# Performance work log

Hardware: AMD Instinct MI355X
Metric: run time of the kernel (lower is better)

Reference implementation:

```python
import jax, jax.numpy as jnp
import numpy as np

WS = 8          # window size
NH = 12         # num heads
DEPTH = 2       # blocks: W-MSA, SW-MSA
EPS = 1e-6
N = WS * WS     # tokens per window


def _rel_index():
    c = np.stack(np.meshgrid(np.arange(WS), np.arange(WS), indexing='ij')).reshape(2, -1)
    rel = (c[:, :, None] - c[:, None, :]).transpose(1, 2, 0)
    rel[:, :, 0] += WS - 1
    rel[:, :, 1] += WS - 1
    rel[:, :, 0] *= 2 * WS - 1
    return rel.sum(-1)  # [N, N] int

REL_IDX = jnp.asarray(_rel_index())


def _shift_mask(H, W, shift):
    # static (numpy) construction, H/W/shift are Python ints
    img = np.zeros((H, W))
    cnt = 0
    for hs in (slice(0, -WS), slice(-WS, -shift), slice(-shift, None)):
        for wsl in (slice(0, -WS), slice(-WS, -shift), slice(-shift, None)):
            img[hs, wsl] = cnt
            cnt += 1
    win = img.reshape(H // WS, WS, W // WS, WS).transpose(0, 2, 1, 3).reshape(-1, N)
    diff = win[:, None, :] - win[:, :, None]
    return jnp.asarray(np.where(diff != 0, -100.0, 0.0), jnp.float32)  # [nW, N, N]


def _ln(x):
    m = x.mean(-1, keepdims=True)
    v = ((x - m) ** 2).mean(-1, keepdims=True)
    return (x - m) * jax.lax.rsqrt(v + EPS)


def _block(x, H, W, emb, p, shift):
    qkv_w, qkv_b, proj_w, proj_b, ff1_w, ff1_b, ff2_w, ff2_b, ada_w, ada_b, bias_table = p
    B, L, C = x.shape
    hd = C // NH
    ada = jax.nn.silu(emb) @ ada_w.T + ada_b  # [B, 6C]
    sh_sa, sc_sa, g_sa, sh_ff, sc_ff, g_ff = jnp.split(ada, 6, axis=-1)
    h = _ln(x) * (1.0 + sc_sa[:, None]) + sh_sa[:, None]
    h = h.reshape(B, H, W, C)
    if shift > 0:
        h = jnp.roll(h, (-shift, -shift), (1, 2))
    # window partition -> [B*nW, N, C]
    win = h.reshape(B, H // WS, WS, W // WS, WS, C).transpose(0, 1, 3, 2, 4, 5).reshape(-1, N, C)
    B_ = win.shape[0]
    qkv = (win @ qkv_w.T + qkv_b).reshape(B_, N, 3, NH, hd)
    q, k, v = qkv[:, :, 0], qkv[:, :, 1], qkv[:, :, 2]
    attn = jnp.einsum('bnhd,bmhd->bhnm', q, k) * (hd ** -0.5)
    bias = bias_table[REL_IDX]  # [N, N, NH]
    attn = attn + bias.transpose(2, 0, 1)[None]
    if shift > 0:
        mask = _shift_mask(H, W, shift)  # [nW, N, N]
        nW = mask.shape[0]
        attn = (attn.reshape(B, nW, NH, N, N) + mask[None, :, None]).reshape(B_, NH, N, N)
    attn = jax.nn.softmax(attn, axis=-1)
    out = jnp.einsum('bhnm,bmhd->bnhd', attn, v).reshape(B_, N, C)
    out = out @ proj_w.T + proj_b
    # window reverse
    h = out.reshape(B, H // WS, W // WS, WS, WS, C).transpose(0, 1, 3, 2, 4, 5).reshape(B, H, W, C)
    if shift > 0:
        h = jnp.roll(h, (shift, shift), (1, 2))
    x = x + g_sa[:, None] * h.reshape(B, L, C)
    h2 = _ln(x) * (1.0 + sc_ff[:, None]) + sh_ff[:, None]
    ff = jax.nn.gelu(h2 @ ff1_w.T + ff1_b, approximate=False) @ ff2_w.T + ff2_b
    return x + g_ff[:, None] * ff


def _forward(x, emb, H, W, params):
    for i in range(DEPTH):
        p = tuple(a[i] for a in params)
        x = _block(x, H, W, emb, p, 0 if i % 2 == 0 else WS // 2)
    return x


def setup_inputs() -> dict:
    key = jax.random.key(0)
    ks = jax.random.split(key, 16)
    C, E, FF = 384, 384, 4 * 384
    B, H, W = 8, 64, 64
    p = lambda k, shape: jax.random.normal(k, shape, jnp.float32) * 0.02
    return {
        'x': jax.random.normal(ks[0], (B, H * W, C), jnp.float32),
        'H': H,
        'W': W,
        'emb': jax.random.normal(ks[1], (B, E), jnp.float32),
        'qkv_w': p(ks[2], (DEPTH, 3 * C, C)),
        'qkv_b': p(ks[3], (DEPTH, 3 * C)),
        'proj_w': p(ks[4], (DEPTH, C, C)),
        'proj_b': p(ks[5], (DEPTH, C)),
        'ff1_w': p(ks[6], (DEPTH, FF, C)),
        'ff1_b': p(ks[7], (DEPTH, FF)),
        'ff2_w': p(ks[8], (DEPTH, C, FF)),
        'ff2_b': p(ks[9], (DEPTH, C)),
        'ada_w': p(ks[10], (DEPTH, 6 * C, E)),
        'ada_b': p(ks[11], (DEPTH, 6 * C)),
        'bias_table': p(ks[12], (DEPTH, (2 * WS - 1) ** 2, NH)),
    }


def reference(x, H, W, emb, qkv_w, qkv_b, proj_w, proj_b, ff1_w, ff1_b, ff2_w, ff2_b, ada_w, ada_b, bias_table):
    params = (qkv_w, qkv_b, proj_w, proj_b, ff1_w, ff1_b, ff2_w, ff2_b, ada_w, ada_b, bias_table)
    return _forward(x, emb, H, W, params)
```

## Files before the change

kernel.cpp:

```cpp
#include <hip/hip_runtime.h>

typedef __bf16 bf16_t;
typedef bf16_t bf16x8 __attribute__((ext_vector_type(8)));
typedef float f32x4 __attribute__((ext_vector_type(4)));

#define EPI_STORE 0
#define EPI_GELU 1
#define EPI_RES_WIN 2
#define EPI_RES_ID 3

__device__ __forceinline__ float bf2f(unsigned short u) {
    union { unsigned int i; float f; } x; x.i = ((unsigned int)u) << 16; return x.f;
}
__device__ __forceinline__ unsigned short f2bf(float f) {
    union { __bf16 h; unsigned short u; } c; c.h = (__bf16)f; return c.u;
}
__device__ __forceinline__ float gelu_f(float v) {
    float u = v * (0.7978845608f + 0.0356774081f * v * v);
    return v / (1.0f + __expf(-2.0f * u));
}

__device__ __forceinline__ void async_cp16(const unsigned short* g, unsigned short* l) {
    __builtin_amdgcn_global_load_lds(
        (const __attribute__((address_space(1))) unsigned int*)g,
        (__attribute__((address_space(3))) unsigned int*)l, 16, 0, 0);
}

__device__ __forceinline__ int map_win(int m, int shift) {
    int n = m & 63, w = m >> 6;
    int b = w >> 6, ww = w & 63;
    int hh = ((ww >> 3) * 8 + (n >> 3) + shift) & 63;
    int wc = ((ww & 7) * 8 + (n & 7) + shift) & 63;
    return (b << 12) + (hh << 6) + wc;
}


__global__ void f2bf_kernel(const float* __restrict__ in,
                            unsigned short* __restrict__ out, int n) {
    int i = blockIdx.x * 256 + threadIdx.x;
    if (i < n) out[i] = f2bf(in[i]);
}

__global__ void silu_kernel(const float* __restrict__ emb,
                            float* __restrict__ out, int n) {
    int i = blockIdx.x * 256 + threadIdx.x;
    if (i < n) { float e = emb[i]; out[i] = e / (1.0f + expf(-e)); }
}

__global__ __launch_bounds__(64) void ada_kernel(
    const float* __restrict__ se,
    const float* __restrict__ ada_w,
    const float* __restrict__ ada_b,
    float* __restrict__ ada_out)
{
    int j = blockIdx.x;
    int layer = blockIdx.y;
    int t = threadIdx.x;
    const float* wr = ada_w + ((long)layer * 2304 + j) * 384;
    float w[6];
#pragma unroll
    for (int q = 0; q < 6; q++) w[q] = wr[t + 64 * q];
    float bias = ada_b[layer * 2304 + j];
    for (int b = 0; b < 8; b++) {
        float p = 0.f;
#pragma unroll
        for (int q = 0; q < 6; q++) p += se[b * 384 + t + 64 * q] * w[q];
#pragma unroll
        for (int o = 32; o > 0; o >>= 1) p += __shfl_xor(p, o);
        if (t == 0) ada_out[((long)layer * 8 + b) * 2304 + j] = p + bias;
    }
}

__global__ __launch_bounds__(256) void ln_mod_kernel(
    const float* __restrict__ x, const float* __restrict__ ada,
    unsigned short* __restrict__ h, int sh_off, int sc_off)
{
    int row = blockIdx.x * 4 + (threadIdx.x >> 6);
    int b = row >> 12;
    int t = threadIdx.x & 63;
    const float* xr = x + (long)row * 384;
    float v[6];
    float s = 0.f;
#pragma unroll
    for (int j = 0; j < 6; j++) { v[j] = xr[t + 64 * j]; s += v[j]; }
#pragma unroll
    for (int o = 32; o > 0; o >>= 1) s += __shfl_xor(s, o);
    float mean = s * (1.0f / 384.0f);
    float s2 = 0.f;
#pragma unroll
    for (int j = 0; j < 6; j++) { float d = v[j] - mean; s2 += d * d; }
#pragma unroll
    for (int o = 32; o > 0; o >>= 1) s2 += __shfl_xor(s2, o);
    float rstd = rsqrtf(s2 * (1.0f / 384.0f) + 1e-6f);
    const float* adab = ada + (long)b * 2304;
#pragma unroll
    for (int j = 0; j < 6; j++) {
        int c = t + 64 * j;
        float val = (v[j] - mean) * rstd * (1.0f + adab[sc_off + c]) + adab[sh_off + c];
        h[(long)row * 384 + c] = f2bf(val);
    }
}


template <int EPI, bool GATHER, bool RESINIT>
__global__ __launch_bounds__(256) void gemm128(
    const unsigned short* __restrict__ A,
    const unsigned short* __restrict__ W,
    const float* __restrict__ bias,
    unsigned short* __restrict__ out,
    float* __restrict__ xres,
    const float* __restrict__ xbase,
    const float* __restrict__ gvec,
    int M, int N, int K, int shift)
{
    __shared__ __align__(16) unsigned short As[128 * 64];
    __shared__ __align__(16) unsigned short Bs[128 * 64];

    const int tid = threadIdx.x;
    const int wv = tid >> 6, lane = tid & 63;
    const int m0 = blockIdx.y * 128, n0 = blockIdx.x * 128;

    const int r8 = lane >> 3;
    const int cofs = ((lane & 7) ^ r8) * 8;
    long arow[4], brow[4];
#pragma unroll
    for (int t = 0; t < 4; t++) {
        int rl = wv * 32 + t * 8 + r8;
        arow[t] = GATHER ? (long)map_win(m0 + rl, shift) : (long)(m0 + rl);
        brow[t] = (long)(n0 + rl);
    }

    const int wm = (wv >> 1) * 64, wn = (wv & 1) * 64;
    const int l16 = lane & 15, quad = lane >> 4;
    const int swz = l16 & 7;

    f32x4 acc[4][4] = {};

    for (int k0 = 0; k0 < K; k0 += 64) {
#pragma unroll
        for (int t = 0; t < 4; t++) {
            async_cp16(A + arow[t] * K + k0 + cofs, As + (wv * 32 + t * 8) * 64);
            async_cp16(W + brow[t] * K + k0 + cofs, Bs + (wv * 32 + t * 8) * 64);
        }
        __syncthreads();

#pragma unroll
        for (int kk = 0; kk < 2; kk++) {
            bf16x8 af[4], bfr[4];
#pragma unroll
            for (int i = 0; i < 4; i++)
                af[i] = *(const bf16x8*)&As[(wm + i * 16 + l16) * 64 +
                                            (((kk * 4 + quad) ^ swz) * 8)];
#pragma unroll
            for (int j = 0; j < 4; j++)
                bfr[j] = *(const bf16x8*)&Bs[(wn + j * 16 + l16) * 64 +
                                             (((kk * 4 + quad) ^ swz) * 8)];
#pragma unroll
            for (int i = 0; i < 4; i++)
#pragma unroll
                for (int j = 0; j < 4; j++)
                    acc[i][j] = __builtin_amdgcn_mfma_f32_16x16x32_bf16(af[i], bfr[j], acc[i][j], 0, 0, 0);
        }
        __syncthreads();
    }

    float bv[4];
#pragma unroll
    for (int j = 0; j < 4; j++) bv[j] = bias[n0 + wn + j * 16 + l16];

#pragma unroll
    for (int i = 0; i < 4; i++) {
#pragma unroll
        for (int r = 0; r < 4; r++) {
            int row = m0 + wm + i * 16 + quad * 4 + r;
            if constexpr (EPI == EPI_STORE || EPI == EPI_GELU) {
                unsigned short* orow = out + (long)row * N + n0 + wn + l16;
#pragma unroll
                for (int j = 0; j < 4; j++) {
                    float v = acc[i][j][r] + bv[j];
                    if constexpr (EPI == EPI_GELU) v = gelu_f(v);
                    orow[j * 16] = f2bf(v);
                }
            } else {
                long dst = (EPI == EPI_RES_WIN) ? (long)map_win(row, shift) : (long)row;
                int b = (int)(dst >> 12);
                float* xrow = xres + dst * 384 + n0 + wn + l16;
                const float* grow = gvec + (long)b * 2304 + n0 + wn + l16;
#pragma unroll
                for (int j = 0; j < 4; j++) {
                    float v = acc[i][j][r] + bv[j];
                    if constexpr (RESINIT) {
                        const float* xbrow = xbase + dst * 384 + n0 + wn + l16;
                        xrow[j * 16] = xbrow[j * 16] + grow[j * 16] * v;
                    } else {
                        xrow[j * 16] += grow[j * 16] * v;
                    }
                }
            }
        }
    }
}


__device__ __forceinline__ int reg3(int p) { return (p < 56) ? 0 : ((p < 60) ? 1 : 2); }

__global__ __launch_bounds__(256) void attn_kernel(
    const unsigned short* __restrict__ qkv,
    const float* __restrict__ bias_table,
    unsigned short* __restrict__ out,
    int shift)
{
    __shared__ unsigned short Pl[4][64 * 68];
    __shared__ unsigned short VTl[4][32 * 68];

    const int wv = threadIdx.x >> 6, lane = threadIdx.x & 63;
    const int head = blockIdx.x * 4 + wv;
    const int win = blockIdx.y;
    const int l16 = lane & 15, quad = lane >> 4;

    unsigned short* P = Pl[wv];
    unsigned short* vt = VTl[wv];

    const long base = (long)win * 64 * 1152 + head * 32;

    bf16x8 qf[4], kf[4];
#pragma unroll
    for (int i = 0; i < 4; i++) {
        qf[i] = *(const bf16x8*)&qkv[base + (long)(i * 16 + l16) * 1152 + quad * 8];
        kf[i] = *(const bf16x8*)&qkv[base + 384 + (long)(i * 16 + l16) * 1152 + quad * 8];
    }
    {
        const uint4* vp = (const uint4*)&qkv[base + 768 + (long)lane * 1152];
#pragma unroll
        for (int c4 = 0; c4 < 4; c4++) {
            uint4 v = vp[c4];
            unsigned int u[4] = {v.x, v.y, v.z, v.w};
#pragma unroll
            for (int e = 0; e < 4; e++) {
                vt[(c4 * 8 + e * 2) * 68 + lane]     = (unsigned short)(u[e] & 0xffffu);
                vt[(c4 * 8 + e * 2 + 1) * 68 + lane] = (unsigned short)(u[e] >> 16);
            }
        }
    }

    f32x4 sacc[4][4] = {};
#pragma unroll
    for (int i = 0; i < 4; i++)
#pragma unroll
        for (int j = 0; j < 4; j++)
            sacc[i][j] = __builtin_amdgcn_mfma_f32_16x16x32_bf16(qf[i], kf[j], sacc[i][j], 0, 0, 0);

    const float scale = 0.17677669529663687f;
    const int ww = win & 63, wi = ww >> 3, wj = ww & 7;

#pragma unroll
    for (int i = 0; i < 4; i++) {
#pragma unroll
        for (int r = 0; r < 4; r++) {
            int n = i * 16 + quad * 4 + r;
            int nr = n >> 3, nc = n & 7;
            int labq = (shift > 0) ? reg3(wi * 8 + nr) * 3 + reg3(wj * 8 + nc) : 0;
            float v[4];
#pragma unroll
            for (int j = 0; j < 4; j++) {
                int m = j * 16 + l16;
                int mr = m >> 3, mc = m & 7;
                float s = sacc[i][j][r] * scale +
                          bias_table[((nr - mr + 7) * 15 + (nc - mc + 7)) * 12 + head];
                if (shift > 0) {
                    int labm = reg3(wi * 8 + mr) * 3 + reg3(wj * 8 + mc);
                    if (labm != labq) s -= 100.0f;
                }
                v[j] = s;
            }
            float mx = fmaxf(fmaxf(v[0], v[1]), fmaxf(v[2], v[3]));
#pragma unroll
            for (int o = 1; o < 16; o <<= 1) mx = fmaxf(mx, __shfl_xor(mx, o));
            float sum = 0.f;
#pragma unroll
            for (int j = 0; j < 4; j++) { v[j] = __expf(v[j] - mx); sum += v[j]; }
#pragma unroll
            for (int o = 1; o < 16; o <<= 1) sum += __shfl_xor(sum, o);
            float inv = 1.0f / sum;
#pragma unroll
            for (int j = 0; j < 4; j++)
                P[n * 68 + j * 16 + l16] = f2bf(v[j] * inv);
        }
    }
    __syncthreads();

    f32x4 oacc[4][2] = {};
#pragma unroll
    for (int kt = 0; kt < 2; kt++) {
        bf16x8 pf[4], vf[2];
#pragma unroll
        for (int i = 0; i < 4; i++)
            pf[i] = *(const bf16x8*)&P[(i * 16 + l16) * 68 + kt * 32 + quad * 8];
#pragma unroll
        for (int jt = 0; jt < 2; jt++)
            vf[jt] = *(const bf16x8*)&vt[(jt * 16 + l16) * 68 + kt * 32 + quad * 8];
#pragma unroll
        for (int i = 0; i < 4; i++)
#pragma unroll
            for (int jt = 0; jt < 2; jt++)
                oacc[i][jt] = __builtin_amdgcn_mfma_f32_16x16x32_bf16(pf[i], vf[jt], oacc[i][jt], 0, 0, 0);
    }

#pragma unroll
    for (int i = 0; i < 4; i++)
#pragma unroll
        for (int jt = 0; jt < 2; jt++)
#pragma unroll
            for (int r = 0; r < 4; r++) {
                int row = i * 16 + quad * 4 + r;
                int col = jt * 16 + l16;
                out[((long)win * 64 + row) * 384 + head * 32 + col] = f2bf(oacc[i][jt][r]);
            }
}


extern "C" void kernel_launch(void* const* d_in, const int* in_sizes, int n_in,
                              void* d_out, int out_size, void* d_ws, size_t ws_size,
                              hipStream_t stream) {
    const float* x_in   = (const float*)d_in[0];
    const float* emb    = (const float*)d_in[3];
    const float* qkv_w  = (const float*)d_in[4];
    const float* qkv_b  = (const float*)d_in[5];
    const float* proj_w = (const float*)d_in[6];
    const float* proj_b = (const float*)d_in[7];
    const float* ff1_w  = (const float*)d_in[8];
    const float* ff1_b  = (const float*)d_in[9];
    const float* ff2_w  = (const float*)d_in[10];
    const float* ff2_b  = (const float*)d_in[11];
    const float* ada_w  = (const float*)d_in[12];
    const float* ada_b  = (const float*)d_in[13];
    const float* bias_t = (const float*)d_in[14];

    char* ws = (char*)d_ws;
    unsigned short* h_buf   = (unsigned short*)ws;
    unsigned short* big_buf = (unsigned short*)(ws + 25165824);
    unsigned short* wqkv    = (unsigned short*)(ws + 125829120);
    unsigned short* wproj   = (unsigned short*)(ws + 127598592);
    unsigned short* wff1    = (unsigned short*)(ws + 128188416);
    unsigned short* wff2    = (unsigned short*)(ws + 130547712);
    float*          ada_out = (float*)(ws + 132907008);
    float*          se      = (float*)(ws + 133054464);

    float* x_acc = (float*)d_out;

    const int M = 32768;

    f2bf_kernel<<<(884736 + 255) / 256, 256, 0, stream>>>(qkv_w, wqkv, 884736);
    f2bf_kernel<<<(294912 + 255) / 256, 256, 0, stream>>>(proj_w, wproj, 294912);
    f2bf_kernel<<<(1179648 + 255) / 256, 256, 0, stream>>>(ff1_w, wff1, 1179648);
    f2bf_kernel<<<(1179648 + 255) / 256, 256, 0, stream>>>(ff2_w, wff2, 1179648);

    silu_kernel<<<(3072 + 255) / 256, 256, 0, stream>>>(emb, se, 3072);
    ada_kernel<<<dim3(2304, 2), 64, 0, stream>>>(se, ada_w, ada_b, ada_out);

    for (int layer = 0; layer < 2; layer++) {
        const int shift = layer ? 4 : 0;
        const float* ada_l = ada_out + (long)layer * 8 * 2304;

        ln_mod_kernel<<<M / 4, 256, 0, stream>>>(layer == 0 ? x_in : x_acc,
                                                 ada_l, h_buf, 0, 384);

        gemm128<EPI_STORE, true, false><<<dim3(9, 256), 256, 0, stream>>>(
            h_buf, wqkv + (long)layer * 1152 * 384, qkv_b + layer * 1152,
            big_buf, nullptr, nullptr, nullptr, M, 1152, 384, shift);

        attn_kernel<<<dim3(3, 512), 256, 0, stream>>>(
            big_buf, bias_t + layer * 225 * 12, h_buf, shift);

        if (layer == 0) {
            gemm128<EPI_RES_WIN, false, true><<<dim3(3, 256), 256, 0, stream>>>(
                h_buf, wproj, proj_b,
                nullptr, x_acc, x_in, ada_l + 768, M, 384, 384, shift);
        } else {
            gemm128<EPI_RES_WIN, false, false><<<dim3(3, 256), 256, 0, stream>>>(
                h_buf, wproj + (long)384 * 384, proj_b + 384,
                nullptr, x_acc, nullptr, ada_l + 768, M, 384, 384, shift);
        }

        ln_mod_kernel<<<M / 4, 256, 0, stream>>>(x_acc, ada_l, h_buf, 1152, 1536);

        gemm128<EPI_GELU, false, false><<<dim3(12, 256), 256, 0, stream>>>(
            h_buf, wff1 + (long)layer * 1536 * 384, ff1_b + layer * 1536,
            big_buf, nullptr, nullptr, nullptr, M, 1536, 384, 0);

        gemm128<EPI_RES_ID, false, false><<<dim3(3, 256), 256, 0, stream>>>(
            big_buf, wff2 + (long)layer * 384 * 1536, ff2_b + layer * 384,
            nullptr, x_acc, nullptr, ada_l + 1920, M, 384, 1536, 0);
    }
}
```

Measured before the change: 771.7 us.

## Stage GEMM epilogue through LDS, remap blocks per XCD, merge weight casts

The GEMM epilogue now writes bf16-rounded results into shared memory and then stores them as coalesced 16-byte rows, replacing scattered 2-byte or 4-byte per-lane writes. Residual epilogues now read the accumulator after bf16 rounding, which changes precision slightly. Block indices are remapped so that each XCD handles a contiguous band of M rows, aiming for better L2 reuse. The four weight-cast launches are merged into one kernel, which relies on the weight buffers being laid out contiguously in the workspace.

Measured after the change: 686.9 us. -11.0%, faster.

```diff
diff --git a/kernel.cpp b/kernel.cpp
--- a/kernel.cpp
+++ b/kernel.cpp
@@ -35,10 +35,16 @@
 }
 
 
-__global__ void f2bf_kernel(const float* __restrict__ in,
-                            unsigned short* __restrict__ out, int n) {
+__global__ void f2bf4_kernel(const float* __restrict__ s0, const float* __restrict__ s1,
+                             const float* __restrict__ s2, const float* __restrict__ s3,
+                             unsigned short* __restrict__ dst) {
     int i = blockIdx.x * 256 + threadIdx.x;
-    if (i < n) out[i] = f2bf(in[i]);
+    const float* s; int off;
+    if (i < 884736)       { s = s0; off = 0; }
+    else if (i < 1179648) { s = s1; off = 884736; }
+    else if (i < 2359296) { s = s2; off = 1179648; }
+    else                  { s = s3; off = 2359296; }
+    dst[i] = f2bf(s[i - off]);
 }
 
 __global__ void silu_kernel(const float* __restrict__ emb,
@@ -113,12 +119,18 @@
     const float* __restrict__ gvec,
     int M, int N, int K, int shift)
 {
-    __shared__ __align__(16) unsigned short As[128 * 64];
-    __shared__ __align__(16) unsigned short Bs[128 * 64];
+    __shared__ __align__(16) unsigned short Sh[17408];
+    unsigned short* As = Sh;
+    unsigned short* Bs = Sh + 8192;
 
     const int tid = threadIdx.x;
     const int wv = tid >> 6, lane = tid & 63;
-    const int m0 = blockIdx.y * 128, n0 = blockIdx.x * 128;
+
+    const int nx = gridDim.x, ny = gridDim.y;
+    const int lin = blockIdx.y * nx + blockIdx.x;
+    const int xcd = lin & 7, p = lin >> 3;
+    const int m0 = (xcd * (ny >> 3) + p / nx) * 128;
+    const int n0 = (p % nx) * 128;
 
     const int r8 = lane >> 3;
     const int cofs = ((lane & 7) ^ r8) * 8;
@@ -168,34 +180,38 @@
 #pragma unroll
     for (int j = 0; j < 4; j++) bv[j] = bias[n0 + wn + j * 16 + l16];
 
-#pragma unroll
-    for (int i = 0; i < 4; i++) {
-#pragma unroll
-        for (int r = 0; r < 4; r++) {
-            int row = m0 + wm + i * 16 + quad * 4 + r;
-            if constexpr (EPI == EPI_STORE || EPI == EPI_GELU) {
-                unsigned short* orow = out + (long)row * N + n0 + wn + l16;
-#pragma unroll
-                for (int j = 0; j < 4; j++) {
-                    float v = acc[i][j][r] + bv[j];
-                    if constexpr (EPI == EPI_GELU) v = gelu_f(v);
-                    orow[j * 16] = f2bf(v);
-                }
-            } else {
-                long dst = (EPI == EPI_RES_WIN) ? (long)map_win(row, shift) : (long)row;
-                int b = (int)(dst >> 12);
-                float* xrow = xres + dst * 384 + n0 + wn + l16;
-                const float* grow = gvec + (long)b * 2304 + n0 + wn + l16;
-#pragma unroll
-                for (int j = 0; j < 4; j++) {
-                    float v = acc[i][j][r] + bv[j];
-                    if constexpr (RESINIT) {
-                        const float* xbrow = xbase + dst * 384 + n0 + wn + l16;
-                        xrow[j * 16] = xbrow[j * 16] + grow[j * 16] * v;
-                    } else {
-                        xrow[j * 16] += grow[j * 16] * v;
-                    }
-                }
+    unsigned short* Cs = Sh;
+#pragma unroll
+    for (int i = 0; i < 4; i++)
+#pragma unroll
+        for (int j = 0; j < 4; j++)
+#pragma unroll
+            for (int r = 0; r < 4; r++) {
+                float v = acc[i][j][r] + bv[j];
+                if constexpr (EPI == EPI_GELU) v = gelu_f(v);
+                Cs[(wm + i * 16 + quad * 4 + r) * 136 + wn + j * 16 + l16] = f2bf(v);
+            }
+    __syncthreads();
+
+#pragma unroll
+    for (int kseg = 0; kseg < 8; kseg++) {
+        int s = tid + 256 * kseg;
+        int row = s >> 4, c8 = (s & 15) << 3;
+        bf16x8 val = *(const bf16x8*)&Cs[row * 136 + c8];
+        if constexpr (EPI == EPI_STORE || EPI == EPI_GELU) {
+            *(bf16x8*)&out[(long)(m0 + row) * N + n0 + c8] = val;
+        } else {
+            long dst = (EPI == EPI_RES_WIN) ? (long)map_win(m0 + row, shift)
+                                            : (long)(m0 + row);
+            float* xrow = xres + dst * 384 + n0 + c8;
+            const float* grow = gvec + (long)(dst >> 12) * 2304 + n0 + c8;
+#pragma unroll
+            for (int e = 0; e < 8; e++) {
+                float v = (float)val[e];
+                float base;
+                if constexpr (RESINIT) base = xbase[dst * 384 + n0 + c8 + e];
+                else                   base = xrow[e];
+                xrow[e] = base + grow[e] * v;
             }
         }
     }
@@ -350,10 +366,7 @@
 
     const int M = 32768;
 
-    f2bf_kernel<<<(884736 + 255) / 256, 256, 0, stream>>>(qkv_w, wqkv, 884736);
-    f2bf_kernel<<<(294912 + 255) / 256, 256, 0, stream>>>(proj_w, wproj, 294912);
-    f2bf_kernel<<<(1179648 + 255) / 256, 256, 0, stream>>>(ff1_w, wff1, 1179648);
-    f2bf_kernel<<<(1179648 + 255) / 256, 256, 0, stream>>>(ff2_w, wff2, 1179648);
+    f2bf4_kernel<<<13824, 256, 0, stream>>>(qkv_w, proj_w, ff1_w, ff2_w, wqkv);
 
     silu_kernel<<<(3072 + 255) / 256, 256, 0, stream>>>(emb, se, 3072);
     ada_kernel<<<dim3(2304, 2), 64, 0, stream>>>(se, ada_w, ada_b, ada_out);
```
